# Performance work log

Hardware: AMD Instinct MI355X
Metric: run time of the kernel (lower is better)

Reference implementation:

```python
import jax, jax.numpy as jnp
import numpy as np

C_S, C_P, FEAT_DIM, NUM_BINS = 256, 128, 64, 22
MAX_DIST = 20.0
C_PAIR_PRE = 20
MAX_LEN = 2056.0


def get_index_embedding(indices, embed_size, max_len=MAX_LEN):
    # indices: (..., ) float; returns (..., embed_size) sinusoidal embedding
    K = jnp.arange(embed_size // 2, dtype=jnp.float32)
    ang = indices[..., None] * jnp.pi / (max_len ** (2.0 * K / embed_size))
    return jnp.concatenate([jnp.sin(ang), jnp.cos(ang)], axis=-1)


def rbf(D, D_min, D_max, D_count):
    # D: (...); returns (..., D_count) Gaussian RBF expansion
    D_mu = jnp.linspace(D_min, D_max, D_count)
    D_sigma = (D_max - D_min) / D_count
    return jnp.exp(-(((D[..., None] - D_mu) / D_sigma) ** 2))


def setup_inputs() -> dict:
    key = jax.random.key(0)
    ks = jax.random.split(key, 12)
    B, L = 1, 512
    total_edge = FEAT_DIM * 3 + NUM_BINS * 2 + C_PAIR_PRE  # 256
    inp = {
        "s": jax.random.normal(ks[0], (B, L, C_S), jnp.float32),
        "t": jax.random.normal(ks[1], (B, L, 3), jnp.float32),
        "sc_t": jax.random.normal(ks[2], (B, L, 3), jnp.float32),
        "pair_repr_pre": jax.random.normal(ks[3], (B, L, L, C_PAIR_PRE), jnp.float32),
        "p_mask": jnp.ones((B, L, L), jnp.float32),
        # linear_s_p: c_s -> feat_dim
        "W_sp": jax.random.normal(ks[4], (FEAT_DIM, C_S), jnp.float32) / np.sqrt(C_S),
        "b_sp": jnp.zeros((FEAT_DIM,), jnp.float32),
        # linear_relpos: feat_dim -> feat_dim
        "W_rp": jax.random.normal(ks[5], (FEAT_DIM, FEAT_DIM), jnp.float32) / np.sqrt(FEAT_DIM),
        "b_rp": jnp.zeros((FEAT_DIM,), jnp.float32),
        # edge_embedder: total_edge -> c_p -> c_p
        "W1": jax.random.normal(ks[6], (C_P, total_edge), jnp.float32) / np.sqrt(total_edge),
        "b1": jnp.zeros((C_P,), jnp.float32),
        "W2": jax.random.normal(ks[7], (C_P, C_P), jnp.float32) / np.sqrt(C_P),
        "b2": jnp.zeros((C_P,), jnp.float32),
    }
    return inp


def reference(s, t, sc_t, pair_repr_pre, p_mask, W_sp, b_sp, W_rp, b_rp, W1, b1, W2, b2):
    B, L, _ = s.shape
    # node projection then pairwise cross-concat -> (B, L, L, 2*feat_dim)
    p_i = jnp.einsum("bld,fd->blf", s, W_sp) + b_sp
    cross = jnp.concatenate([
        jnp.broadcast_to(p_i[:, :, None, :], (B, L, L, FEAT_DIM)),
        jnp.broadcast_to(p_i[:, None, :, :], (B, L, L, FEAT_DIM)),
    ], axis=-1)
    # relative-position sinusoidal embedding -> linear
    pos = jnp.arange(L, dtype=jnp.float32)[None, :]  # (1, L) broadcast over batch
    rel_pos = pos[:, :, None] - pos[:, None, :]      # (1, L, L)
    rel_pos = jnp.broadcast_to(rel_pos, (B, L, L))
    pos_emb = get_index_embedding(rel_pos, FEAT_DIM)
    relpos_feats = jnp.einsum("bijf,gf->bijg", pos_emb, W_rp) + b_rp
    # RBF distance expansions for backbone (t) and sidechain (sc_t) coords
    d_t = jnp.linalg.norm(t[:, :, None, :] - t[:, None, :, :], axis=-1)
    dist_feats = rbf(d_t, 0.0, MAX_DIST, NUM_BINS)
    d_sc = jnp.linalg.norm(sc_t[:, :, None, :] - sc_t[:, None, :, :], axis=-1)
    sc_feats = rbf(d_sc, 0.0, MAX_DIST, NUM_BINS)
    all_edge = jnp.concatenate([cross, relpos_feats, dist_feats, sc_feats, pair_repr_pre], axis=-1)
    # 2-layer MLP (dropout = 0 / eval mode)
    h = jax.nn.relu(jnp.einsum("bije,pe->bijp", all_edge, W1) + b1)
    edge_feats = jnp.einsum("bijp,qp->bijq", h, W2) + b2
    return edge_feats
```

## Files before the change

### kernel.cpp

```cpp
#include <hip/hip_runtime.h>
#include <hip/hip_bf16.h>


typedef __attribute__((ext_vector_type(8))) short v8s;
typedef __attribute__((ext_vector_type(4))) float v4f;

#define PI_F 3.14159265358979323846f

__global__ __launch_bounds__(64) void precompute_kernel(
    const float* __restrict__ s, const float* __restrict__ W_sp,
    const float* __restrict__ b_sp, const float* __restrict__ W_rp,
    const float* __restrict__ b_rp, const float* __restrict__ W1,
    const float* __restrict__ W2,
    __hip_bfloat16* __restrict__ p_bf, __hip_bfloat16* __restrict__ relT,
    __hip_bfloat16* __restrict__ W1b, __hip_bfloat16* __restrict__ W2b)
{
    const int b = blockIdx.x;
    const int tid = threadIdx.x;

    if (b < 512) {
        __shared__ float srow[256];
        #pragma unroll
        for (int k = 0; k < 4; k++) srow[k * 64 + tid] = s[b * 256 + k * 64 + tid];
        __syncthreads();
        float acc = b_sp[tid];
        const float* w = W_sp + tid * 256;
        #pragma unroll 8
        for (int d = 0; d < 256; d++) acc += srow[d] * w[d];
        p_bf[b * 64 + tid] = __float2bfloat16(acc);
    } else if (b < 1535) {
        const int didx = b - 512;
        const float rel = (float)(didx - 511);
        __shared__ float femb[64];
        const int K = tid & 31;
        const float freq = powf(2056.0f, (2.0f * (float)K) / 64.0f);
        const float ang = rel * PI_F / freq;
        femb[tid] = (tid < 32) ? sinf(ang) : cosf(ang);
        __syncthreads();
        float acc = b_rp[tid];
        const float* w = W_rp + tid * 64;
        #pragma unroll
        for (int f = 0; f < 64; f++) acc += femb[f] * w[f];
        relT[didx * 64 + tid] = __float2bfloat16(acc);
    } else {
        const int base = (b - 1535) * 512 + tid;
        #pragma unroll
        for (int k = 0; k < 8; k++) {
            int e = base + k * 64;
            if (e < 32768) W1b[e] = __float2bfloat16(W1[e]);
            else           W2b[e - 32768] = __float2bfloat16(W2[e - 32768]);
        }
    }
}

__global__ __launch_bounds__(256, 3) void edge_main(
    const float* __restrict__ t3, const float* __restrict__ sc3,
    const float* __restrict__ pre,
    const float* __restrict__ b1, const float* __restrict__ b2,
    const __hip_bfloat16* __restrict__ p_bf, const __hip_bfloat16* __restrict__ relT,
    const __hip_bfloat16* __restrict__ W1b, const __hip_bfloat16* __restrict__ W2b,
    float* __restrict__ out)
{
    __shared__ __hip_bfloat16 Ash[64][264];
    __shared__ __hip_bfloat16 Hsh[64][136];
    __shared__ float dtv[64];
    __shared__ float dsv[64];

    const int tid = threadIdx.x;
    const int blk = blockIdx.x;
    const int i  = blk >> 3;
    const int j0 = (blk & 7) << 6;

    if (tid < 128) {
        const int r = tid & 63;
        const float* base = (tid < 64) ? t3 : sc3;
        const float dx = base[i * 3 + 0] - base[(j0 + r) * 3 + 0];
        const float dy = base[i * 3 + 1] - base[(j0 + r) * 3 + 1];
        const float dz = base[i * 3 + 2] - base[(j0 + r) * 3 + 2];
        const float d = sqrtf(dx * dx + dy * dy + dz * dz);
        if (tid < 64) dtv[r] = d; else dsv[r] = d;
    }

    for (int c = tid; c < 64 * 8; c += 256) {
        const int r = c >> 3;
        const int cc = (c & 7) << 3;
        *(uint4*)&Ash[r][cc]       = *(const uint4*)&p_bf[i * 64 + cc];
        *(uint4*)&Ash[r][64 + cc]  = *(const uint4*)&p_bf[(j0 + r) * 64 + cc];
        *(uint4*)&Ash[r][128 + cc] = *(const uint4*)&relT[(i - (j0 + r) + 511) * 64 + cc];
    }
    for (int c = tid; c < 64 * 5; c += 256) {
        const int r = c / 5;
        const int f4 = (c % 5) * 4;
        const float4 v = *(const float4*)&pre[(i * 512 + j0 + r) * 20 + f4];
        Ash[r][236 + f4 + 0] = __float2bfloat16(v.x);
        Ash[r][236 + f4 + 1] = __float2bfloat16(v.y);
        Ash[r][236 + f4 + 2] = __float2bfloat16(v.z);
        Ash[r][236 + f4 + 3] = __float2bfloat16(v.w);
    }
    __syncthreads();
    for (int c = tid; c < 64 * 44; c += 256) {
        const int r = c / 44;
        const int f = c % 44;
        const float d = (f < 22) ? dtv[r] : dsv[r];
        const int m = (f < 22) ? f : f - 22;
        const float x = (d - (float)m * (20.0f / 21.0f)) * 1.1f;
        Ash[r][192 + f] = __float2bfloat16(__expf(-x * x));
    }
    __syncthreads();

    const int wv   = tid >> 6;
    const int lane = tid & 63;
    const int l16  = lane & 15;
    const int quad = lane >> 4;
    const int nbase = wv * 32;

    float b1v0 = b1[nbase + l16],      b1v1 = b1[nbase + 16 + l16];
    float b2v0 = b2[nbase + l16],      b2v1 = b2[nbase + 16 + l16];

    v4f acc[4][2];
    #pragma unroll
    for (int s4 = 0; s4 < 4; s4++)
        #pragma unroll
        for (int n = 0; n < 2; n++) acc[s4][n] = (v4f){0.f, 0.f, 0.f, 0.f};

    const __hip_bfloat16* w1r0 = W1b + (nbase + l16) * 256 + quad * 8;
    const __hip_bfloat16* w1r1 = w1r0 + 16 * 256;

    #pragma unroll
    for (int kt = 0; kt < 8; kt++) {
        const int ko = kt * 32 + quad * 8;
        v8s a0 = *(const v8s*)&Ash[ 0 + l16][ko];
        v8s a1 = *(const v8s*)&Ash[16 + l16][ko];
        v8s a2 = *(const v8s*)&Ash[32 + l16][ko];
        v8s a3 = *(const v8s*)&Ash[48 + l16][ko];
        v8s bb0 = *(const v8s*)(w1r0 + kt * 32);
        v8s bb1 = *(const v8s*)(w1r1 + kt * 32);
        acc[0][0] = __builtin_amdgcn_mfma_f32_16x16x32_bf16(a0, bb0, acc[0][0], 0, 0, 0);
        acc[1][0] = __builtin_amdgcn_mfma_f32_16x16x32_bf16(a1, bb0, acc[1][0], 0, 0, 0);
        acc[2][0] = __builtin_amdgcn_mfma_f32_16x16x32_bf16(a2, bb0, acc[2][0], 0, 0, 0);
        acc[3][0] = __builtin_amdgcn_mfma_f32_16x16x32_bf16(a3, bb0, acc[3][0], 0, 0, 0);
        acc[0][1] = __builtin_amdgcn_mfma_f32_16x16x32_bf16(a0, bb1, acc[0][1], 0, 0, 0);
        acc[1][1] = __builtin_amdgcn_mfma_f32_16x16x32_bf16(a1, bb1, acc[1][1], 0, 0, 0);
        acc[2][1] = __builtin_amdgcn_mfma_f32_16x16x32_bf16(a2, bb1, acc[2][1], 0, 0, 0);
        acc[3][1] = __builtin_amdgcn_mfma_f32_16x16x32_bf16(a3, bb1, acc[3][1], 0, 0, 0);
    }

    #pragma unroll
    for (int s4 = 0; s4 < 4; s4++) {
        #pragma unroll
        for (int n = 0; n < 2; n++) {
            const float bv = n ? b1v1 : b1v0;
            #pragma unroll
            for (int r = 0; r < 4; r++) {
                float v = acc[s4][n][r] + bv;
                v = fmaxf(v, 0.0f);
                Hsh[s4 * 16 + quad * 4 + r][nbase + n * 16 + l16] = __float2bfloat16(v);
            }
        }
    }
    __syncthreads();

    v4f acc2[4][2];
    #pragma unroll
    for (int s4 = 0; s4 < 4; s4++)
        #pragma unroll
        for (int n = 0; n < 2; n++) acc2[s4][n] = (v4f){0.f, 0.f, 0.f, 0.f};

    const __hip_bfloat16* w2r0 = W2b + (nbase + l16) * 128 + quad * 8;
    const __hip_bfloat16* w2r1 = w2r0 + 16 * 128;

    #pragma unroll
    for (int kt = 0; kt < 4; kt++) {
        const int ko = kt * 32 + quad * 8;
        v8s a0 = *(const v8s*)&Hsh[ 0 + l16][ko];
        v8s a1 = *(const v8s*)&Hsh[16 + l16][ko];
        v8s a2 = *(const v8s*)&Hsh[32 + l16][ko];
        v8s a3 = *(const v8s*)&Hsh[48 + l16][ko];
        v8s bb0 = *(const v8s*)(w2r0 + kt * 32);
        v8s bb1 = *(const v8s*)(w2r1 + kt * 32);
        acc2[0][0] = __builtin_amdgcn_mfma_f32_16x16x32_bf16(a0, bb0, acc2[0][0], 0, 0, 0);
        acc2[1][0] = __builtin_amdgcn_mfma_f32_16x16x32_bf16(a1, bb0, acc2[1][0], 0, 0, 0);
        acc2[2][0] = __builtin_amdgcn_mfma_f32_16x16x32_bf16(a2, bb0, acc2[2][0], 0, 0, 0);
        acc2[3][0] = __builtin_amdgcn_mfma_f32_16x16x32_bf16(a3, bb0, acc2[3][0], 0, 0, 0);
        acc2[0][1] = __builtin_amdgcn_mfma_f32_16x16x32_bf16(a0, bb1, acc2[0][1], 0, 0, 0);
        acc2[1][1] = __builtin_amdgcn_mfma_f32_16x16x32_bf16(a1, bb1, acc2[1][1], 0, 0, 0);
        acc2[2][1] = __builtin_amdgcn_mfma_f32_16x16x32_bf16(a2, bb1, acc2[2][1], 0, 0, 0);
        acc2[3][1] = __builtin_amdgcn_mfma_f32_16x16x32_bf16(a3, bb1, acc2[3][1], 0, 0, 0);
    }

    const int rowbase = blk * 64;
    #pragma unroll
    for (int s4 = 0; s4 < 4; s4++) {
        #pragma unroll
        for (int n = 0; n < 2; n++) {
            const float bv = n ? b2v1 : b2v0;
            const int col = nbase + n * 16 + l16;
            #pragma unroll
            for (int r = 0; r < 4; r++) {
                const int row = rowbase + s4 * 16 + quad * 4 + r;
                out[row * 128 + col] = acc2[s4][n][r] + bv;
            }
        }
    }
}

extern "C" void kernel_launch(void* const* d_in, const int* in_sizes, int n_in,
                              void* d_out, int out_size, void* d_ws, size_t ws_size,
                              hipStream_t stream) {
    const float* s    = (const float*)d_in[0];
    const float* t3   = (const float*)d_in[1];
    const float* sc3  = (const float*)d_in[2];
    const float* pre  = (const float*)d_in[3];
    const float* W_sp = (const float*)d_in[5];
    const float* b_sp = (const float*)d_in[6];
    const float* W_rp = (const float*)d_in[7];
    const float* b_rp = (const float*)d_in[8];
    const float* W1   = (const float*)d_in[9];
    const float* b1   = (const float*)d_in[10];
    const float* W2   = (const float*)d_in[11];
    const float* b2   = (const float*)d_in[12];
    float* out = (float*)d_out;

    char* ws = (char*)d_ws;
    __hip_bfloat16* p_bf = (__hip_bfloat16*)(ws);
    __hip_bfloat16* relT = (__hip_bfloat16*)(ws + 65536);
    __hip_bfloat16* W1b  = (__hip_bfloat16*)(ws + 65536 + 131072);
    __hip_bfloat16* W2b  = (__hip_bfloat16*)(ws + 65536 + 131072 + 65536);

    precompute_kernel<<<1631, 64, 0, stream>>>(s, W_sp, b_sp, W_rp, b_rp, W1, W2,
                                               p_bf, relT, W1b, W2b);
    edge_main<<<4096, 256, 0, stream>>>(t3, sc3, pre, b1, b2,
                                        p_bf, relT, W1b, W2b, out);
}
```

Measured before the change: 231.6 us.

## Restructure precompute blocks, alias LDS buffers, and coalesce output stores via shared memory

Precompute now uses 256-thread blocks that each handle several rows and stage transposed weights in LDS, and the weight conversion uses float4 loads. The main kernel aliases Ash, Hsh and an output staging buffer in one LDS allocation so more blocks fit per CU (launch bounds raised to 4). It merges the distance and RBF computation into one pass, removing a barrier, and prefetches the first weight fragments early. Output goes through LDS so global stores are full float4 rows rather than scattered scalars. The price is extra barriers and LDS traffic in the epilogue.

```diff
diff --git a/kernel.cpp b/kernel.cpp
--- a/kernel.cpp
+++ b/kernel.cpp
@@ -7,7 +7,7 @@
 
 #define PI_F 3.14159265358979323846f
 
-__global__ __launch_bounds__(64) void precompute_kernel(
+__global__ __launch_bounds__(256) void precompute_kernel(
     const float* __restrict__ s, const float* __restrict__ W_sp,
     const float* __restrict__ b_sp, const float* __restrict__ W_rp,
     const float* __restrict__ b_rp, const float* __restrict__ W1,
@@ -17,43 +17,81 @@
 {
     const int b = blockIdx.x;
     const int tid = threadIdx.x;
-
-    if (b < 512) {
-        __shared__ float srow[256];
-        #pragma unroll
-        for (int k = 0; k < 4; k++) srow[k * 64 + tid] = s[b * 256 + k * 64 + tid];
+    __shared__ float lds[128 * 65 + 8 * 256];
+
+    if (b < 64) {
+        float* Wt   = lds;
+        float* srow = lds + 128 * 65;
+        const int row0 = b * 8;
+        const int f  = tid & 63;
+        const int rh = tid >> 6;
+        #pragma unroll
+        for (int k = 0; k < 8; k++) {
+            const int idx = tid + 256 * k;
+            const int r = idx >> 8, d = idx & 255;
+            srow[r * 256 + d] = s[(row0 + r) * 256 + d];
+        }
+        float acc0 = b_sp[f];
+        float acc1 = acc0;
+        for (int pass = 0; pass < 2; pass++) {
+            __syncthreads();
+            #pragma unroll
+            for (int k = 0; k < 32; k++) {
+                const int idx = tid + 256 * k;
+                const int fs = idx >> 7, ds = idx & 127;
+                Wt[ds * 65 + fs] = W_sp[fs * 256 + pass * 128 + ds];
+            }
+            __syncthreads();
+            #pragma unroll 4
+            for (int d = 0; d < 128; d++) {
+                const float w = Wt[d * 65 + f];
+                acc0 += srow[rh * 256 + pass * 128 + d] * w;
+                acc1 += srow[(rh + 4) * 256 + pass * 128 + d] * w;
+            }
+        }
+        p_bf[(row0 + rh) * 64 + f]     = __float2bfloat16(acc0);
+        p_bf[(row0 + rh + 4) * 64 + f] = __float2bfloat16(acc1);
+    } else if (b < 320) {
+        float* WrT  = lds;
+        float* femb = lds + 64 * 65;
+        const int r0 = (b - 64) * 4;
+        #pragma unroll
+        for (int k = 0; k < 16; k++) {
+            const int idx = tid + 256 * k;
+            const int g = idx >> 6, ff = idx & 63;
+            WrT[ff * 65 + g] = W_rp[g * 64 + ff];
+        }
+        {
+            const int r = tid >> 6, c = tid & 63;
+            const float rel = (float)(r0 + r - 511);
+            const int K = c & 31;
+            const float freq = powf(2056.0f, (2.0f * (float)K) / 64.0f);
+            const float ang = rel * PI_F / freq;
+            femb[r * 64 + c] = (c < 32) ? sinf(ang) : cosf(ang);
+        }
         __syncthreads();
-        float acc = b_sp[tid];
-        const float* w = W_sp + tid * 256;
-        #pragma unroll 8
-        for (int d = 0; d < 256; d++) acc += srow[d] * w[d];
-        p_bf[b * 64 + tid] = __float2bfloat16(acc);
-    } else if (b < 1535) {
-        const int didx = b - 512;
-        const float rel = (float)(didx - 511);
-        __shared__ float femb[64];
-        const int K = tid & 31;
-        const float freq = powf(2056.0f, (2.0f * (float)K) / 64.0f);
-        const float ang = rel * PI_F / freq;
-        femb[tid] = (tid < 32) ? sinf(ang) : cosf(ang);
-        __syncthreads();
-        float acc = b_rp[tid];
-        const float* w = W_rp + tid * 64;
-        #pragma unroll
-        for (int f = 0; f < 64; f++) acc += femb[f] * w[f];
-        relT[didx * 64 + tid] = __float2bfloat16(acc);
+        const int g = tid & 63, r = tid >> 6;
+        float acc = b_rp[g];
+        #pragma unroll
+        for (int ff = 0; ff < 64; ff++) acc += femb[r * 64 + ff] * WrT[ff * 65 + g];
+        relT[(r0 + r) * 64 + g] = __float2bfloat16(acc);
     } else {
-        const int base = (b - 1535) * 512 + tid;
-        #pragma unroll
-        for (int k = 0; k < 8; k++) {
-            int e = base + k * 64;
-            if (e < 32768) W1b[e] = __float2bfloat16(W1[e]);
-            else           W2b[e - 32768] = __float2bfloat16(W2[e - 32768]);
+        #pragma unroll
+        for (int k = 0; k < 2; k++) {
+            const int idx4 = (b - 320) * 512 + k * 256 + tid;
+            const int e = idx4 * 4;
+            const float4 v = (e < 32768) ? *(const float4*)&W1[e]
+                                         : *(const float4*)&W2[e - 32768];
+            __hip_bfloat16* dst = (e < 32768) ? (W1b + e) : (W2b + (e - 32768));
+            dst[0] = __float2bfloat16(v.x);
+            dst[1] = __float2bfloat16(v.y);
+            dst[2] = __float2bfloat16(v.z);
+            dst[3] = __float2bfloat16(v.w);
         }
     }
 }
 
-__global__ __launch_bounds__(256, 3) void edge_main(
+__global__ __launch_bounds__(256, 4) void edge_main(
     const float* __restrict__ t3, const float* __restrict__ sc3,
     const float* __restrict__ pre,
     const float* __restrict__ b1, const float* __restrict__ b2,
@@ -61,80 +99,88 @@
     const __hip_bfloat16* __restrict__ W1b, const __hip_bfloat16* __restrict__ W2b,
     float* __restrict__ out)
 {
-    __shared__ __hip_bfloat16 Ash[64][264];
-    __shared__ __hip_bfloat16 Hsh[64][136];
-    __shared__ float dtv[64];
-    __shared__ float dsv[64];
+    __shared__ char smem[64 * 264 * 2];
+    __hip_bfloat16 (*Ash)[264] = (__hip_bfloat16(*)[264])smem;
+    __hip_bfloat16 (*Hsh)[136] = (__hip_bfloat16(*)[136])smem;
+    float          (*Cf)[132]  = (float(*)[132])smem;
 
     const int tid = threadIdx.x;
     const int blk = blockIdx.x;
     const int i  = blk >> 3;
     const int j0 = (blk & 7) << 6;
 
-    if (tid < 128) {
-        const int r = tid & 63;
-        const float* base = (tid < 64) ? t3 : sc3;
-        const float dx = base[i * 3 + 0] - base[(j0 + r) * 3 + 0];
-        const float dy = base[i * 3 + 1] - base[(j0 + r) * 3 + 1];
-        const float dz = base[i * 3 + 2] - base[(j0 + r) * 3 + 2];
-        const float d = sqrtf(dx * dx + dy * dy + dz * dz);
-        if (tid < 64) dtv[r] = d; else dsv[r] = d;
-    }
-
-    for (int c = tid; c < 64 * 8; c += 256) {
+    const int wv   = tid >> 6;
+    const int lane = tid & 63;
+    const int l16  = lane & 15;
+    const int quad = lane >> 4;
+    const int nbase = wv * 32;
+
+    const float b1v0 = b1[nbase + l16],      b1v1 = b1[nbase + 16 + l16];
+    const float b2v0 = b2[nbase + l16],      b2v1 = b2[nbase + 16 + l16];
+    const __hip_bfloat16* w1r0 = W1b + (nbase + l16) * 256 + quad * 8;
+    const __hip_bfloat16* w1r1 = w1r0 + 16 * 256;
+    const __hip_bfloat16* w2r0 = W2b + (nbase + l16) * 128 + quad * 8;
+    const __hip_bfloat16* w2r1 = w2r0 + 16 * 128;
+    const v8s p10 = *(const v8s*)w1r0;
+    const v8s p11 = *(const v8s*)w1r1;
+    const v8s p20 = *(const v8s*)w2r0;
+    const v8s p21 = *(const v8s*)w2r1;
+
+    #pragma unroll
+    for (int c = tid; c < 512; c += 256) {
         const int r = c >> 3;
         const int cc = (c & 7) << 3;
         *(uint4*)&Ash[r][cc]       = *(const uint4*)&p_bf[i * 64 + cc];
         *(uint4*)&Ash[r][64 + cc]  = *(const uint4*)&p_bf[(j0 + r) * 64 + cc];
         *(uint4*)&Ash[r][128 + cc] = *(const uint4*)&relT[(i - (j0 + r) + 511) * 64 + cc];
     }
-    for (int c = tid; c < 64 * 5; c += 256) {
+    for (int c = tid; c < 320; c += 256) {
         const int r = c / 5;
         const int f4 = (c % 5) * 4;
-        const float4 v = *(const float4*)&pre[(i * 512 + j0 + r) * 20 + f4];
+        const float4 v = *(const float4*)&pre[((size_t)i * 512 + j0 + r) * 20 + f4];
         Ash[r][236 + f4 + 0] = __float2bfloat16(v.x);
         Ash[r][236 + f4 + 1] = __float2bfloat16(v.y);
         Ash[r][236 + f4 + 2] = __float2bfloat16(v.z);
         Ash[r][236 + f4 + 3] = __float2bfloat16(v.w);
     }
-    __syncthreads();
-    for (int c = tid; c < 64 * 44; c += 256) {
-        const int r = c / 44;
-        const int f = c % 44;
-        const float d = (f < 22) ? dtv[r] : dsv[r];
-        const int m = (f < 22) ? f : f - 22;
-        const float x = (d - (float)m * (20.0f / 21.0f)) * 1.1f;
-        Ash[r][192 + f] = __float2bfloat16(__expf(-x * x));
-    }
-    __syncthreads();
-
-    const int wv   = tid >> 6;
-    const int lane = tid & 63;
-    const int l16  = lane & 15;
-    const int quad = lane >> 4;
-    const int nbase = wv * 32;
-
-    float b1v0 = b1[nbase + l16],      b1v1 = b1[nbase + 16 + l16];
-    float b2v0 = b2[nbase + l16],      b2v1 = b2[nbase + 16 + l16];
+    {
+        const int r = tid >> 2;
+        const int fo = (tid & 3) * 11;
+        const int j = j0 + r;
+        const float dxt = t3[i * 3 + 0] - t3[j * 3 + 0];
+        const float dyt = t3[i * 3 + 1] - t3[j * 3 + 1];
+        const float dzt = t3[i * 3 + 2] - t3[j * 3 + 2];
+        const float dt = sqrtf(dxt * dxt + dyt * dyt + dzt * dzt);
+        const float dxs = sc3[i * 3 + 0] - sc3[j * 3 + 0];
+        const float dys = sc3[i * 3 + 1] - sc3[j * 3 + 1];
+        const float dzs = sc3[i * 3 + 2] - sc3[j * 3 + 2];
+        const float ds = sqrtf(dxs * dxs + dys * dys + dzs * dzs);
+        #pragma unroll
+        for (int q = 0; q < 11; q++) {
+            const int f = fo + q;
+            const float d = (f < 22) ? dt : ds;
+            const int m = (f < 22) ? f : f - 22;
+            const float x = (d - (float)m * (20.0f / 21.0f)) * 1.1f;
+            Ash[r][192 + f] = __float2bfloat16(__expf(-x * x));
+        }
+    }
+    __syncthreads();
 
     v4f acc[4][2];
     #pragma unroll
     for (int s4 = 0; s4 < 4; s4++)
         #pragma unroll
         for (int n = 0; n < 2; n++) acc[s4][n] = (v4f){0.f, 0.f, 0.f, 0.f};
-
-    const __hip_bfloat16* w1r0 = W1b + (nbase + l16) * 256 + quad * 8;
-    const __hip_bfloat16* w1r1 = w1r0 + 16 * 256;
 
     #pragma unroll
     for (int kt = 0; kt < 8; kt++) {
         const int ko = kt * 32 + quad * 8;
-        v8s a0 = *(const v8s*)&Ash[ 0 + l16][ko];
-        v8s a1 = *(const v8s*)&Ash[16 + l16][ko];
-        v8s a2 = *(const v8s*)&Ash[32 + l16][ko];
-        v8s a3 = *(const v8s*)&Ash[48 + l16][ko];
-        v8s bb0 = *(const v8s*)(w1r0 + kt * 32);
-        v8s bb1 = *(const v8s*)(w1r1 + kt * 32);
+        const v8s a0 = *(const v8s*)&Ash[ 0 + l16][ko];
+        const v8s a1 = *(const v8s*)&Ash[16 + l16][ko];
+        const v8s a2 = *(const v8s*)&Ash[32 + l16][ko];
+        const v8s a3 = *(const v8s*)&Ash[48 + l16][ko];
+        const v8s bb0 = (kt == 0) ? p10 : *(const v8s*)(w1r0 + kt * 32);
+        const v8s bb1 = (kt == 0) ? p11 : *(const v8s*)(w1r1 + kt * 32);
         acc[0][0] = __builtin_amdgcn_mfma_f32_16x16x32_bf16(a0, bb0, acc[0][0], 0, 0, 0);
         acc[1][0] = __builtin_amdgcn_mfma_f32_16x16x32_bf16(a1, bb0, acc[1][0], 0, 0, 0);
         acc[2][0] = __builtin_amdgcn_mfma_f32_16x16x32_bf16(a2, bb0, acc[2][0], 0, 0, 0);
@@ -144,6 +190,7 @@
         acc[2][1] = __builtin_amdgcn_mfma_f32_16x16x32_bf16(a2, bb1, acc[2][1], 0, 0, 0);
         acc[3][1] = __builtin_amdgcn_mfma_f32_16x16x32_bf16(a3, bb1, acc[3][1], 0, 0, 0);
     }
+    __syncthreads();
 
     #pragma unroll
     for (int s4 = 0; s4 < 4; s4++) {
@@ -166,18 +213,15 @@
         #pragma unroll
         for (int n = 0; n < 2; n++) acc2[s4][n] = (v4f){0.f, 0.f, 0.f, 0.f};
 
-    const __hip_bfloat16* w2r0 = W2b + (nbase + l16) * 128 + quad * 8;
-    const __hip_bfloat16* w2r1 = w2r0 + 16 * 128;
-
     #pragma unroll
     for (int kt = 0; kt < 4; kt++) {
         const int ko = kt * 32 + quad * 8;
-        v8s a0 = *(const v8s*)&Hsh[ 0 + l16][ko];
-        v8s a1 = *(const v8s*)&Hsh[16 + l16][ko];
-        v8s a2 = *(const v8s*)&Hsh[32 + l16][ko];
-        v8s a3 = *(const v8s*)&Hsh[48 + l16][ko];
-        v8s bb0 = *(const v8s*)(w2r0 + kt * 32);
-        v8s bb1 = *(const v8s*)(w2r1 + kt * 32);
+        const v8s a0 = *(const v8s*)&Hsh[ 0 + l16][ko];
+        const v8s a1 = *(const v8s*)&Hsh[16 + l16][ko];
+        const v8s a2 = *(const v8s*)&Hsh[32 + l16][ko];
+        const v8s a3 = *(const v8s*)&Hsh[48 + l16][ko];
+        const v8s bb0 = (kt == 0) ? p20 : *(const v8s*)(w2r0 + kt * 32);
+        const v8s bb1 = (kt == 0) ? p21 : *(const v8s*)(w2r1 + kt * 32);
         acc2[0][0] = __builtin_amdgcn_mfma_f32_16x16x32_bf16(a0, bb0, acc2[0][0], 0, 0, 0);
         acc2[1][0] = __builtin_amdgcn_mfma_f32_16x16x32_bf16(a1, bb0, acc2[1][0], 0, 0, 0);
         acc2[2][0] = __builtin_amdgcn_mfma_f32_16x16x32_bf16(a2, bb0, acc2[2][0], 0, 0, 0);
@@ -187,8 +231,8 @@
         acc2[2][1] = __builtin_amdgcn_mfma_f32_16x16x32_bf16(a2, bb1, acc2[2][1], 0, 0, 0);
         acc2[3][1] = __builtin_amdgcn_mfma_f32_16x16x32_bf16(a3, bb1, acc2[3][1], 0, 0, 0);
     }
-
-    const int rowbase = blk * 64;
+    __syncthreads();
+
     #pragma unroll
     for (int s4 = 0; s4 < 4; s4++) {
         #pragma unroll
@@ -197,10 +241,19 @@
             const int col = nbase + n * 16 + l16;
             #pragma unroll
             for (int r = 0; r < 4; r++) {
-                const int row = rowbase + s4 * 16 + quad * 4 + r;
-                out[row * 128 + col] = acc2[s4][n][r] + bv;
-            }
-        }
+                Cf[s4 * 16 + quad * 4 + r][col] = acc2[s4][n][r] + bv;
+            }
+        }
+    }
+    __syncthreads();
+
+    const size_t rowbase = (size_t)blk * 64;
+    #pragma unroll
+    for (int k = 0; k < 8; k++) {
+        const int q = tid + k * 256;
+        const int row = q >> 5;
+        const int c4 = (q & 31) * 4;
+        *(float4*)&out[(rowbase + row) * 128 + c4] = *(const float4*)&Cf[row][c4];
     }
 }
 
@@ -227,7 +280,7 @@
     __hip_bfloat16* W1b  = (__hip_bfloat16*)(ws + 65536 + 131072);
     __hip_bfloat16* W2b  = (__hip_bfloat16*)(ws + 65536 + 131072 + 65536);
 
-    precompute_kernel<<<1631, 64, 0, stream>>>(s, W_sp, b_sp, W_rp, b_rp, W1, W2,
+    precompute_kernel<<<344, 256, 0, stream>>>(s, W_sp, b_sp, W_rp, b_rp, W1, W2,
                                                p_bf, relT, W1b, W2b);
     edge_main<<<4096, 256, 0, stream>>>(t3, sc3, pre, b1, b2,
                                         p_bf, relT, W1b, W2b, out);
```

Result: faster. 219.3 us (-5.3%).
